# Kernel optimization log

Measured on AMD Instinct MI355X. Metric: run time of the kernel, lower is better.

Reference implementation:

```python
import jax, jax.numpy as jnp
import numpy as np


def _relative_position_index(ws: int) -> np.ndarray:
    # Matches torch meshgrid (ij) construction in _init_relative_positions.
    coords = np.stack(np.meshgrid(np.arange(ws), np.arange(ws), indexing='ij'), axis=0).reshape(2, -1)  # [2, ws*ws]
    rel = coords[:, :, None] - coords[:, None, :]          # [2, N, N]
    rel = rel.transpose(1, 2, 0).copy()                    # [N, N, 2]
    rel[:, :, 0] += ws - 1
    rel[:, :, 1] += ws - 1
    rel[:, :, 0] *= 2 * ws - 1
    return rel.sum(-1)                                     # [N, N] int


def setup_inputs() -> dict:
    key = jax.random.key(0)
    ks = jax.random.split(key, 6)
    B, N, C, H, WS = 4096, 49, 512, 16, 7
    x = jax.random.normal(ks[0], (B, N, C), dtype=jnp.float32)
    w_qkv = jax.random.normal(ks[1], (C, 3 * C), dtype=jnp.float32) * (C ** -0.5)
    b_qkv = jax.random.normal(ks[2], (3 * C,), dtype=jnp.float32) * 0.02
    w_proj = jax.random.normal(ks[3], (C, C), dtype=jnp.float32) * (C ** -0.5)
    b_proj = jax.random.normal(ks[4], (C,), dtype=jnp.float32) * 0.02
    bias_table = jax.random.normal(ks[5], ((2 * WS - 1) ** 2, H), dtype=jnp.float32) * 0.02
    return {"x": x, "w_qkv": w_qkv, "b_qkv": b_qkv, "w_proj": w_proj,
            "b_proj": b_proj, "bias_table": bias_table,
            "num_heads": H, "window_size": WS}


def reference(x, w_qkv, b_qkv, w_proj, b_proj, bias_table, num_heads, window_size):
    B, N, C = x.shape
    hd = C // num_heads
    qkv = (x @ w_qkv + b_qkv).reshape(B, N, 3, num_heads, hd)
    q, k, v = (qkv[:, :, i].transpose(0, 2, 1, 3) for i in range(3))  # each [B, H, N, hd]
    # NOTE: scale uses full channel dim C (as in source), not head_dim.
    attn = jnp.einsum('bhnd,bhmd->bhnm', q, k) * (C ** -0.5)          # [B, H, N, N]
    idx = _relative_position_index(window_size)                        # [N, N] static
    rel_bias = bias_table[idx].transpose(2, 0, 1)                      # [H, N, N]
    attn = jax.nn.softmax(attn + rel_bias[None], axis=-1)
    out = jnp.einsum('bhnm,bhmd->bhnd', attn, v)                       # [B, H, N, hd]
    out = out.transpose(0, 2, 1, 3).reshape(B, N, C)
    return out @ w_proj + b_proj
```

## Files before the change

### kernel.cpp

```cpp
#include <hip/hip_runtime.h>
#include <hip/hip_bf16.h>

typedef __attribute__((ext_vector_type(8))) short bf16x8;
typedef __attribute__((ext_vector_type(4))) float f32x4;

#define DEVI __device__ __forceinline__

DEVI short f2bf(float f) {
  union { float f; unsigned u; } v; v.f = f;
  unsigned r = v.u + 0x7FFFu + ((v.u >> 16) & 1u);
  return (short)(r >> 16);
}

DEVI void gl16(const void* g, void* l) {
  __builtin_amdgcn_global_load_lds((const __attribute__((address_space(1))) unsigned*)g,
                                   (__attribute__((address_space(3))) unsigned*)l,
                                   16, 0, 0);
}

DEVI float exp2a(float x) { float r; asm("v_exp_f32 %0, %1" : "=v"(r) : "v"(x)); return r; }

DEVI unsigned pk2(float lo, float hi) {
  union { __hip_bfloat162 h; unsigned u; } v;
  float2 f; f.x = lo; f.y = hi;
  v.h = __float22bfloat162_rn(f);
  return v.u;
}

union U8 { unsigned u[4]; bf16x8 v; };
DEVI bf16x8 mk8(unsigned a, unsigned b, unsigned c, unsigned d) {
  U8 x; x.u[0]=a; x.u[1]=b; x.u[2]=c; x.u[3]=d; return x.v;
}


__global__ __launch_bounds__(256) void conv_x_k(const float* __restrict__ x,
                                                short* __restrict__ xb) {
  long i = (long)blockIdx.x * 256 + threadIdx.x;
  const float4* xf = (const float4*)x;
  float4 a = xf[i * 2], c = xf[i * 2 + 1];
  bf16x8 r;
  r[0] = f2bf(a.x); r[1] = f2bf(a.y); r[2] = f2bf(a.z); r[3] = f2bf(a.w);
  r[4] = f2bf(c.x); r[5] = f2bf(c.y); r[6] = f2bf(c.z); r[7] = f2bf(c.w);
  *(bf16x8*)(xb + i * 8) = r;
}

__global__ __launch_bounds__(256) void prep_k(const float* __restrict__ wq,
                                              const float* __restrict__ wp,
                                              const float* __restrict__ btab,
                                              short* __restrict__ wqT,
                                              short* __restrict__ wpT,
                                              float* __restrict__ biasT) {
  int bid = blockIdx.x;
  if (bid < 3072) {
    int i = bid * 256 + threadIdx.x;
    int n = i >> 9, k = i & 511;
    wqT[i] = f2bf(wq[k * 1536 + n]);
  } else if (bid < 4096) {
    int i = (bid - 3072) * 256 + threadIdx.x;
    int n = i >> 9, k = i & 511;
    wpT[i] = f2bf(wp[k * 512 + n]);
  } else {
    int i = (bid - 4096) * 256 + threadIdx.x;
    int h = i >> 12, m = (i >> 6) & 63, n = i & 63;
    float v;
    if (m >= 49) {
      v = -1e30f;
    } else {
      int nn = n > 48 ? 48 : n;
      int ni = nn / 7, nj = nn - ni * 7;
      int mi = m / 7,  mj = m - mi * 7;
      int idx = (ni - mi + 6) * 13 + (nj - mj + 6);
      v = btab[idx * 16 + h] * 1.4426950408889634f;
    }
    biasT[i] = v;
  }
}


template <int EPI>
__global__ __launch_bounds__(512, 2)
void gemm256(const short* __restrict__ A, const short* __restrict__ Bt,
             const float* __restrict__ bias, void* __restrict__ outp, int ctiles) {
  __shared__ short Ls[65536];

  const int nwg = gridDim.x;
  const int w = blockIdx.x;
  const int chunk = nwg >> 3;
  const int tid = (w & 7) * chunk + (w >> 3);
  const int rt = tid / ctiles, ct = tid % ctiles;
  const long m0 = (long)rt * 256;
  const int n0 = ct * 256;

  const int t = threadIdx.x;
  const int lane = t & 63;
  const int wv = t >> 6;
  const int wr = wv >> 2;
  const int wc = wv & 3;
  const int l15 = lane & 15, g = lane >> 4, g4 = g * 4;

  const int gch = (t & 3) ^ ((t >> 3) & 3);
  const short* Ag = A + (m0 + (t >> 2)) * 512 + gch * 8;
  const short* Bg = Bt + (long)(n0 + (t >> 2)) * 512 + gch * 8;

  const int cA = ((g ^ ((l15 >> 1) & 3))) * 8;
  const int rowA = (wr * 128 + l15) * 32;
  const int rowB = (wc * 64 + l15) * 32;

  f32x4 acc[8][4] = {};
  bf16x8 af[8], bfr[2];

#define STAGE_A(ktn, kh, bufn)                                         \
  { const short* s_ = Ag + (ktn) * 64 + (kh) * 32;                     \
    short* d_ = (bufn) + (kh) * 8192 + t * 8;                          \
    gl16(s_, d_); gl16(s_ + 128 * 512, d_ + 4096); }
#define STAGE_B(ktn, kh, bufn)                                         \
  { const short* s_ = Bg + (ktn) * 64 + (kh) * 32;                     \
    short* d_ = (bufn) + 16384 + (kh) * 8192 + t * 8;                  \
    gl16(s_, d_); gl16(s_ + 128 * 512, d_ + 4096); }
#define LOAD_AF(Ab, kh)                                                \
  _Pragma("unroll")                                                    \
  for (int mf = 0; mf < 8; ++mf)                                       \
    af[mf] = *(const bf16x8*)((Ab) + (kh) * 8192 + rowA + mf * 512 + cA);
#define LOAD_BF(Ab, kh, nh)                                            \
  bfr[0] = *(const bf16x8*)((Ab) + 16384 + (kh) * 8192 + rowB + ((nh) * 2) * 512 + cA); \
  bfr[1] = *(const bf16x8*)((Ab) + 16384 + (kh) * 8192 + rowB + ((nh) * 2 + 1) * 512 + cA);
#define MFMA16(nh)                                                     \
  __builtin_amdgcn_s_setprio(1);                                       \
  _Pragma("unroll")                                                    \
  for (int mf = 0; mf < 8; ++mf) {                                     \
    acc[mf][(nh) * 2] = __builtin_amdgcn_mfma_f32_16x16x32_bf16(af[mf], bfr[0], acc[mf][(nh) * 2], 0, 0, 0);         \
    acc[mf][(nh) * 2 + 1] = __builtin_amdgcn_mfma_f32_16x16x32_bf16(af[mf], bfr[1], acc[mf][(nh) * 2 + 1], 0, 0, 0); \
  }                                                                    \
  __builtin_amdgcn_s_setprio(0);
#define BAR() asm volatile("s_barrier" ::: "memory")
#define VMW4() asm volatile("s_waitcnt vmcnt(4)" ::: "memory")

  STAGE_A(0, 0, Ls); STAGE_B(0, 0, Ls); STAGE_A(0, 1, Ls); STAGE_B(0, 1, Ls);
  VMW4();
  BAR();

  for (int kt = 0; kt < 8; ++kt) {
    const short* Ab = Ls + (kt & 1) * 32768;
    short* Bn = Ls + ((kt & 1) ^ 1) * 32768;
    const int ktn = kt < 7 ? kt + 1 : 7;

    LOAD_AF(Ab, 0); LOAD_BF(Ab, 0, 0);
    STAGE_A(ktn, 0, Bn);
    BAR(); MFMA16(0); BAR();

    LOAD_BF(Ab, 0, 1);
    STAGE_B(ktn, 0, Bn);
    VMW4();
    BAR(); MFMA16(1); BAR();

    LOAD_AF(Ab, 1); LOAD_BF(Ab, 1, 0);
    STAGE_A(ktn, 1, Bn);
    BAR(); MFMA16(0); BAR();

    LOAD_BF(Ab, 1, 1);
    STAGE_B(ktn, 1, Bn);
    VMW4();
    BAR(); MFMA16(1); BAR();
  }

  if (EPI == 0) {
    __syncthreads();
#pragma unroll
    for (int mf = 0; mf < 8; ++mf)
#pragma unroll
      for (int r = 0; r < 4; ++r) {
        int lrow = wr * 128 + mf * 16 + g4 + r;
#pragma unroll
        for (int nf = 0; nf < 4; ++nf) {
          int lcol = wc * 64 + nf * 16 + l15;
          Ls[lrow * 256 + lcol] = f2bf(acc[mf][nf][r] + bias[n0 + lcol]);
        }
      }
    __syncthreads();
    short* qkv = (short*)outp;
    const int cq = n0 >> 8;
    const int ii = cq >> 1;
#pragma unroll
    for (int s = 0; s < 16; ++s) {
      int c = s * 512 + t;
      int row = c >> 5, sub = c & 31;
      int hl = sub >> 2, d0 = (sub & 3) * 8;
      int rg = (int)m0 + row;
      int b = rg / 49, n = rg - b * 49;
      int h = (cq & 1) * 8 + hl;
      long dst = (long)((b * 16 + h) * 3 + ii) * 1568 + n * 32 + d0;
      *(bf16x8*)(qkv + dst) = *(const bf16x8*)(Ls + row * 256 + hl * 32 + d0);
    }
  } else {
    __syncthreads();
    float* out = (float*)outp;
#pragma unroll
    for (int mf = 0; mf < 8; ++mf)
#pragma unroll
      for (int r = 0; r < 4; ++r) {
        long row = m0 + wr * 128 + mf * 16 + g4 + r;
#pragma unroll
        for (int nf = 0; nf < 4; ++nf) {
          int col = n0 + wc * 64 + nf * 16 + l15;
          out[row * 512 + col] = acc[mf][nf][r] + bias[col];
        }
      }
  }
#undef STAGE_A
#undef STAGE_B
#undef LOAD_AF
#undef LOAD_BF
#undef MFMA16
#undef BAR
#undef VMW4
}


__global__ __launch_bounds__(256, 3)
void attn49(const short* __restrict__ qkvb, const float* __restrict__ biasT,
            short* __restrict__ ao) {
  __shared__ short Vl[4][2048];

  const int t = threadIdx.x, lane = t & 63, wv = t >> 6;
  const int l15 = lane & 15, g = lane >> 4, g4 = g * 4;
  const int b = blockIdx.x >> 2;
  const int h = (blockIdx.x & 3) * 4 + wv;

  const short* qb = qkvb + (long)(b * 16 + h) * 3 * 1568;
  const short* kb = qb + 1568;
  const short* vb = kb + 1568;
  short* Vs = Vl[wv];

#pragma unroll
  for (int it = 0; it < 4; ++it) {
    int c = it * 64 + lane; c = c > 195 ? 195 : c;
    *(bf16x8*)(Vs + c * 8) = *(const bf16x8*)(vb + c * 8);
  }

  bf16x8 qf[4], kf[4];
#pragma unroll
  for (int i = 0; i < 4; ++i) {
    int row = i * 16 + l15; row = row > 48 ? 48 : row;
    kf[i] = *(const bf16x8*)(kb + row * 32 + g * 8);
    qf[i] = *(const bf16x8*)(qb + row * 32 + g * 8);
  }

  f32x4 s[4][4] = {};
#pragma unroll
  for (int i = 0; i < 4; ++i)
#pragma unroll
    for (int j = 0; j < 4; ++j)
      s[i][j] = __builtin_amdgcn_mfma_f32_16x16x32_bf16(kf[i], qf[j], s[i][j], 0, 0, 0);

  bf16x8 vf[2][2];
#pragma unroll
  for (int kt = 0; kt < 2; ++kt)
#pragma unroll
    for (int hi = 0; hi < 2; ++hi)
#pragma unroll
      for (int r = 0; r < 4; ++r) {
        int m = kt * 32 + hi * 16 + g4 + r;
        m = m > 48 ? 48 : m;
#pragma unroll
        for (int dt = 0; dt < 2; ++dt)
          vf[kt][dt][hi * 4 + r] = Vs[m * 32 + dt * 16 + l15];
      }

  const float* biasH = biasT + h * 4096;
  float sum[4] = {0.f, 0.f, 0.f, 0.f};
#pragma unroll
  for (int i = 0; i < 4; ++i)
#pragma unroll
    for (int r = 0; r < 4; ++r) {
      int m = i * 16 + g4 + r;
      const float* bp = biasH + m * 64 + l15;
#pragma unroll
      for (int j = 0; j < 4; ++j) {
        float p = exp2a(fmaf(s[i][j][r], 0.06375871f, bp[j * 16]));
        s[i][j][r] = p;
        sum[j] += p;
      }
    }
#pragma unroll
  for (int j = 0; j < 4; ++j) {
    sum[j] += __shfl_xor(sum[j], 16);
    sum[j] += __shfl_xor(sum[j], 32);
    sum[j] = 1.f / sum[j];
  }

  unsigned pk[4][4][2];
#pragma unroll
  for (int j = 0; j < 4; ++j)
#pragma unroll
    for (int i = 0; i < 4; ++i) {
      pk[j][i][0] = pk2(s[i][j][0] * sum[j], s[i][j][1] * sum[j]);
      pk[j][i][1] = pk2(s[i][j][2] * sum[j], s[i][j][3] * sum[j]);
    }

  f32x4 o[4][2] = {};
#pragma unroll
  for (int j = 0; j < 4; ++j) {
    bf16x8 a0 = mk8(pk[j][0][0], pk[j][0][1], pk[j][1][0], pk[j][1][1]);
    bf16x8 a1 = mk8(pk[j][2][0], pk[j][2][1], pk[j][3][0], pk[j][3][1]);
    o[j][0] = __builtin_amdgcn_mfma_f32_16x16x32_bf16(a0, vf[0][0], o[j][0], 0, 0, 0);
    o[j][0] = __builtin_amdgcn_mfma_f32_16x16x32_bf16(a1, vf[1][0], o[j][0], 0, 0, 0);
    o[j][1] = __builtin_amdgcn_mfma_f32_16x16x32_bf16(a0, vf[0][1], o[j][1], 0, 0, 0);
    o[j][1] = __builtin_amdgcn_mfma_f32_16x16x32_bf16(a1, vf[1][1], o[j][1], 0, 0, 0);
  }

#pragma unroll
  for (int j = 0; j < 4; ++j)
#pragma unroll
    for (int r = 0; r < 4; ++r) {
      int n = j * 16 + g4 + r;
      if (n < 49) {
        long off = ((long)b * 49 + n) * 512 + h * 32 + l15;
        ao[off]      = f2bf(o[j][0][r]);
        ao[off + 16] = f2bf(o[j][1][r]);
      }
    }
}


extern "C" void kernel_launch(void* const* d_in, const int* in_sizes, int n_in,
                              void* d_out, int out_size, void* d_ws, size_t ws_size,
                              hipStream_t stream) {
  (void)in_sizes; (void)n_in; (void)ws_size;
  const float* x      = (const float*)d_in[0];
  const float* w_qkv  = (const float*)d_in[1];
  const float* b_qkv  = (const float*)d_in[2];
  const float* w_proj = (const float*)d_in[3];
  const float* b_proj = (const float*)d_in[4];
  const float* btab   = (const float*)d_in[5];

  char* ws = (char*)d_ws;
  short* xb  = (short*)ws;
  short* wqT = (short*)(ws + 205520896L);
  short* wpT = (short*)(ws + 205520896L + 1572864L);
  short* qkv = (short*)(ws + 205520896L + 1572864L + 524288L);
  short* ao  = xb;
  float* biasT = (float*)d_out + (out_size - 65536);

  conv_x_k<<<50176, 256, 0, stream>>>(x, xb);
  prep_k  <<<4352, 256, 0, stream>>>(w_qkv, w_proj, btab, wqT, wpT, biasT);
  gemm256<0><<<4704, 512, 0, stream>>>(xb, wqT, b_qkv, (void*)qkv, 6);
  attn49  <<<16384, 256, 0, stream>>>(qkv, biasT, ao);
  gemm256<1><<<1568, 512, 0, stream>>>(ao, wpT, b_proj, d_out, 2);
}
```

Baseline: 881.4 us.

## Fuse fp32-to-bf16 conversion of x into QKV GEMM and preswizzle weights

Removes the separate conversion kernel that turned x into bf16. The QKV GEMM now loads fp32 x directly, converts it in registers and writes it to LDS. Weights are prepacked into an MFMA fragment layout so B operands come straight from global/L2 into registers, freeing LDS for A only. The main loop is restructured with register-staged A loads, fewer barriers and halved LDS buffers. In exchange the fp32 A loads double global traffic per tile, the staging uses more registers, and the occupancy hint of 2 is dropped.

```diff
diff --git a/kernel.cpp b/kernel.cpp
--- a/kernel.cpp
+++ b/kernel.cpp
@@ -5,17 +5,12 @@
 typedef __attribute__((ext_vector_type(4))) float f32x4;
 
 #define DEVI __device__ __forceinline__
+#define MFMA __builtin_amdgcn_mfma_f32_16x16x32_bf16
 
 DEVI short f2bf(float f) {
   union { float f; unsigned u; } v; v.f = f;
   unsigned r = v.u + 0x7FFFu + ((v.u >> 16) & 1u);
   return (short)(r >> 16);
-}
-
-DEVI void gl16(const void* g, void* l) {
-  __builtin_amdgcn_global_load_lds((const __attribute__((address_space(1))) unsigned*)g,
-                                   (__attribute__((address_space(3))) unsigned*)l,
-                                   16, 0, 0);
 }
 
 DEVI float exp2a(float x) { float r; asm("v_exp_f32 %0, %1" : "=v"(r) : "v"(x)); return r; }
@@ -32,33 +27,20 @@
   U8 x; x.u[0]=a; x.u[1]=b; x.u[2]=c; x.u[3]=d; return x.v;
 }
 
-
-__global__ __launch_bounds__(256) void conv_x_k(const float* __restrict__ x,
-                                                short* __restrict__ xb) {
-  long i = (long)blockIdx.x * 256 + threadIdx.x;
-  const float4* xf = (const float4*)x;
-  float4 a = xf[i * 2], c = xf[i * 2 + 1];
-  bf16x8 r;
-  r[0] = f2bf(a.x); r[1] = f2bf(a.y); r[2] = f2bf(a.z); r[3] = f2bf(a.w);
-  r[4] = f2bf(c.x); r[5] = f2bf(c.y); r[6] = f2bf(c.z); r[7] = f2bf(c.w);
-  *(bf16x8*)(xb + i * 8) = r;
-}
-
 __global__ __launch_bounds__(256) void prep_k(const float* __restrict__ wq,
                                               const float* __restrict__ wp,
                                               const float* __restrict__ btab,
-                                              short* __restrict__ wqT,
-                                              short* __restrict__ wpT,
+                                              short* __restrict__ wqP,
+                                              short* __restrict__ wpP,
                                               float* __restrict__ biasT) {
   int bid = blockIdx.x;
-  if (bid < 3072) {
-    int i = bid * 256 + threadIdx.x;
-    int n = i >> 9, k = i & 511;
-    wqT[i] = f2bf(wq[k * 1536 + n]);
-  } else if (bid < 4096) {
-    int i = (bid - 3072) * 256 + threadIdx.x;
-    int n = i >> 9, k = i & 511;
-    wpT[i] = f2bf(wp[k * 512 + n]);
+  if (bid < 4096) {
+    int i = (bid < 3072 ? bid : bid - 3072) * 256 + threadIdx.x;
+    int e = i & 7, lane = (i >> 3) & 63, kc = (i >> 9) & 15, cf = i >> 13;
+    int k = kc * 32 + (lane >> 4) * 8 + e;
+    int col = cf * 16 + (lane & 15);
+    if (bid < 3072) wqP[i] = f2bf(wq[k * 1536 + col]);
+    else            wpP[i] = f2bf(wp[k * 512 + col]);
   } else {
     int i = (bid - 4096) * 256 + threadIdx.x;
     int h = i >> 12, m = (i >> 6) & 63, n = i & 63;
@@ -77,9 +59,9 @@
 }
 
 
-template <int EPI>
-__global__ __launch_bounds__(512, 2)
-void gemm256(const short* __restrict__ A, const short* __restrict__ Bt,
+template <int EPI, bool AF32>
+__global__ __launch_bounds__(512)
+void gemm256(const void* __restrict__ Ap, const short* __restrict__ wB,
              const float* __restrict__ bias, void* __restrict__ outp, int ctiles) {
   __shared__ short Ls[65536];
 
@@ -99,68 +81,87 @@
   const int l15 = lane & 15, g = lane >> 4, g4 = g * 4;
 
   const int gch = (t & 3) ^ ((t >> 3) & 3);
-  const short* Ag = A + (m0 + (t >> 2)) * 512 + gch * 8;
-  const short* Bg = Bt + (long)(n0 + (t >> 2)) * 512 + gch * 8;
-
-  const int cA = ((g ^ ((l15 >> 1) & 3))) * 8;
+  const float* Agf = (const float*)Ap + (m0 + (t >> 2)) * 512 + gch * 8;
+  const short* Agh = (const short*)Ap + (m0 + (t >> 2)) * 512 + gch * 8;
+
+  const int cA = (g ^ ((l15 >> 1) & 3)) * 8;
   const int rowA = (wr * 128 + l15) * 32;
-  const int rowB = (wc * 64 + l15) * 32;
+
+  const short* wBb = wB + ((long)(ct * 16 + wc * 4) << 13) + lane * 8;
 
   f32x4 acc[8][4] = {};
-  bf16x8 af[8], bfr[2];
-
-#define STAGE_A(ktn, kh, bufn)                                         \
-  { const short* s_ = Ag + (ktn) * 64 + (kh) * 32;                     \
-    short* d_ = (bufn) + (kh) * 8192 + t * 8;                          \
-    gl16(s_, d_); gl16(s_ + 128 * 512, d_ + 4096); }
-#define STAGE_B(ktn, kh, bufn)                                         \
-  { const short* s_ = Bg + (ktn) * 64 + (kh) * 32;                     \
-    short* d_ = (bufn) + 16384 + (kh) * 8192 + t * 8;                  \
-    gl16(s_, d_); gl16(s_ + 128 * 512, d_ + 4096); }
-#define LOAD_AF(Ab, kh)                                                \
-  _Pragma("unroll")                                                    \
-  for (int mf = 0; mf < 8; ++mf)                                       \
-    af[mf] = *(const bf16x8*)((Ab) + (kh) * 8192 + rowA + mf * 512 + cA);
-#define LOAD_BF(Ab, kh, nh)                                            \
-  bfr[0] = *(const bf16x8*)((Ab) + 16384 + (kh) * 8192 + rowB + ((nh) * 2) * 512 + cA); \
-  bfr[1] = *(const bf16x8*)((Ab) + 16384 + (kh) * 8192 + rowB + ((nh) * 2 + 1) * 512 + cA);
-#define MFMA16(nh)                                                     \
-  __builtin_amdgcn_s_setprio(1);                                       \
-  _Pragma("unroll")                                                    \
-  for (int mf = 0; mf < 8; ++mf) {                                     \
-    acc[mf][(nh) * 2] = __builtin_amdgcn_mfma_f32_16x16x32_bf16(af[mf], bfr[0], acc[mf][(nh) * 2], 0, 0, 0);         \
-    acc[mf][(nh) * 2 + 1] = __builtin_amdgcn_mfma_f32_16x16x32_bf16(af[mf], bfr[1], acc[mf][(nh) * 2 + 1], 0, 0, 0); \
-  }                                                                    \
+  bf16x8 af[8];
+  bf16x8 bP[4][2];
+  float4 ga[4][2];
+  bf16x8 gb[4];
+
+#define ISSUE_A(ktn)                                                          \
+  if (AF32) {                                                                 \
+    _Pragma("unroll")                                                         \
+    for (int c = 0; c < 4; ++c) {                                             \
+      const float* s_ = Agf + (c >> 1) * 65536 + (c & 1) * 32 + (ktn) * 64;   \
+      ga[c][0] = *(const float4*)s_;                                          \
+      ga[c][1] = *(const float4*)(s_ + 4);                                    \
+    }                                                                         \
+  } else {                                                                    \
+    _Pragma("unroll")                                                         \
+    for (int c = 0; c < 4; ++c)                                               \
+      gb[c] = *(const bf16x8*)(Agh + (c >> 1) * 65536 + (c & 1) * 32 + (ktn) * 64); \
+  }
+#define WRITE_A(nb)                                                           \
+  _Pragma("unroll")                                                           \
+  for (int c = 0; c < 4; ++c) {                                               \
+    short* d_ = (nb) + (c & 1) * 8192 + (c >> 1) * 4096 + t * 8;              \
+    if (AF32) {                                                               \
+      *(bf16x8*)d_ = mk8(pk2(ga[c][0].x, ga[c][0].y), pk2(ga[c][0].z, ga[c][0].w), \
+                         pk2(ga[c][1].x, ga[c][1].y), pk2(ga[c][1].z, ga[c][1].w)); \
+    } else {                                                                  \
+      *(bf16x8*)d_ = gb[c];                                                   \
+    }                                                                         \
+  }
+#define LOAD_BP(p, ktn)                                                       \
+  bP[p][0] = *(const bf16x8*)(wBb + ((((((p) & 1) * 2 + 0) * 16 + ((ktn) * 2 + ((p) >> 1)))) << 9)); \
+  bP[p][1] = *(const bf16x8*)(wBb + ((((((p) & 1) * 2 + 1) * 16 + ((ktn) * 2 + ((p) >> 1)))) << 9));
+#define LOAD_AF(buf, kh)                                                      \
+  _Pragma("unroll")                                                           \
+  for (int mf = 0; mf < 8; ++mf)                                              \
+    af[mf] = *(const bf16x8*)((buf) + (kh) * 8192 + rowA + mf * 512 + cA);
+#define MFMA16(p)                                                             \
+  __builtin_amdgcn_s_setprio(1);                                              \
+  _Pragma("unroll")                                                           \
+  for (int mf = 0; mf < 8; ++mf) {                                            \
+    acc[mf][((p) & 1) * 2]     = MFMA(af[mf], bP[p][0], acc[mf][((p) & 1) * 2], 0, 0, 0);     \
+    acc[mf][((p) & 1) * 2 + 1] = MFMA(af[mf], bP[p][1], acc[mf][((p) & 1) * 2 + 1], 0, 0, 0); \
+  }                                                                           \
   __builtin_amdgcn_s_setprio(0);
 #define BAR() asm volatile("s_barrier" ::: "memory")
-#define VMW4() asm volatile("s_waitcnt vmcnt(4)" ::: "memory")
-
-  STAGE_A(0, 0, Ls); STAGE_B(0, 0, Ls); STAGE_A(0, 1, Ls); STAGE_B(0, 1, Ls);
-  VMW4();
+
+  ISSUE_A(0);
+  asm volatile("s_waitcnt vmcnt(0)" ::: "memory");
+  WRITE_A(Ls);
+  LOAD_BP(0, 0); LOAD_BP(1, 0); LOAD_BP(2, 0); LOAD_BP(3, 0);
+  asm volatile("s_waitcnt lgkmcnt(0)" ::: "memory");
   BAR();
 
   for (int kt = 0; kt < 8; ++kt) {
-    const short* Ab = Ls + (kt & 1) * 32768;
-    short* Bn = Ls + ((kt & 1) ^ 1) * 32768;
-    const int ktn = kt < 7 ? kt + 1 : 7;
-
-    LOAD_AF(Ab, 0); LOAD_BF(Ab, 0, 0);
-    STAGE_A(ktn, 0, Bn);
-    BAR(); MFMA16(0); BAR();
-
-    LOAD_BF(Ab, 0, 1);
-    STAGE_B(ktn, 0, Bn);
-    VMW4();
-    BAR(); MFMA16(1); BAR();
-
-    LOAD_AF(Ab, 1); LOAD_BF(Ab, 1, 0);
-    STAGE_A(ktn, 1, Bn);
-    BAR(); MFMA16(0); BAR();
-
-    LOAD_BF(Ab, 1, 1);
-    STAGE_B(ktn, 1, Bn);
-    VMW4();
-    BAR(); MFMA16(1); BAR();
+    const short* buf = Ls + (kt & 1) * 16384;
+    short* nb = Ls + ((kt & 1) ^ 1) * 16384;
+
+    LOAD_AF(buf, 0);
+    if (kt < 7) ISSUE_A(kt + 1);
+    MFMA16(0);
+    MFMA16(1);
+    LOAD_AF(buf, 1);
+    if (kt < 7) { LOAD_BP(0, kt + 1); LOAD_BP(1, kt + 1); }
+    MFMA16(2);
+    if (kt < 7) {
+      asm volatile("s_waitcnt vmcnt(4)" ::: "memory");
+      WRITE_A(nb);
+    }
+    MFMA16(3);
+    if (kt < 7) { LOAD_BP(2, kt + 1); LOAD_BP(3, kt + 1); }
+    asm volatile("s_waitcnt lgkmcnt(0)" ::: "memory");
+    BAR();
   }
 
   if (EPI == 0) {
@@ -192,7 +193,6 @@
       *(bf16x8*)(qkv + dst) = *(const bf16x8*)(Ls + row * 256 + hl * 32 + d0);
     }
   } else {
-    __syncthreads();
     float* out = (float*)outp;
 #pragma unroll
     for (int mf = 0; mf < 8; ++mf)
@@ -206,13 +206,12 @@
         }
       }
   }
-#undef STAGE_A
-#undef STAGE_B
+#undef ISSUE_A
+#undef WRITE_A
+#undef LOAD_BP
 #undef LOAD_AF
-#undef LOAD_BF
 #undef MFMA16
 #undef BAR
-#undef VMW4
 }
 
 
@@ -250,7 +249,7 @@
   for (int i = 0; i < 4; ++i)
 #pragma unroll
     for (int j = 0; j < 4; ++j)
-      s[i][j] = __builtin_amdgcn_mfma_f32_16x16x32_bf16(kf[i], qf[j], s[i][j], 0, 0, 0);
+      s[i][j] = MFMA(kf[i], qf[j], s[i][j], 0, 0, 0);
 
   bf16x8 vf[2][2];
 #pragma unroll
@@ -302,10 +301,10 @@
   for (int j = 0; j < 4; ++j) {
     bf16x8 a0 = mk8(pk[j][0][0], pk[j][0][1], pk[j][1][0], pk[j][1][1]);
     bf16x8 a1 = mk8(pk[j][2][0], pk[j][2][1], pk[j][3][0], pk[j][3][1]);
-    o[j][0] = __builtin_amdgcn_mfma_f32_16x16x32_bf16(a0, vf[0][0], o[j][0], 0, 0, 0);
-    o[j][0] = __builtin_amdgcn_mfma_f32_16x16x32_bf16(a1, vf[1][0], o[j][0], 0, 0, 0);
-    o[j][1] = __builtin_amdgcn_mfma_f32_16x16x32_bf16(a0, vf[0][1], o[j][1], 0, 0, 0);
-    o[j][1] = __builtin_amdgcn_mfma_f32_16x16x32_bf16(a1, vf[1][1], o[j][1], 0, 0, 0);
+    o[j][0] = MFMA(a0, vf[0][0], o[j][0], 0, 0, 0);
+    o[j][0] = MFMA(a1, vf[1][0], o[j][0], 0, 0, 0);
+    o[j][1] = MFMA(a0, vf[0][1], o[j][1], 0, 0, 0);
+    o[j][1] = MFMA(a1, vf[1][1], o[j][1], 0, 0, 0);
   }
 
 #pragma unroll
@@ -334,16 +333,14 @@
   const float* btab   = (const float*)d_in[5];
 
   char* ws = (char*)d_ws;
-  short* xb  = (short*)ws;
-  short* wqT = (short*)(ws + 205520896L);
-  short* wpT = (short*)(ws + 205520896L + 1572864L);
-  short* qkv = (short*)(ws + 205520896L + 1572864L + 524288L);
-  short* ao  = xb;
+  short* wqP = (short*)ws;
+  short* wpP = (short*)(ws + 1572864L);
+  short* qkv = (short*)(ws + 2097152L);
+  short* ao  = (short*)(ws + 2097152L + 616562688L);
   float* biasT = (float*)d_out + (out_size - 65536);
 
-  conv_x_k<<<50176, 256, 0, stream>>>(x, xb);
-  prep_k  <<<4352, 256, 0, stream>>>(w_qkv, w_proj, btab, wqT, wpT, biasT);
-  gemm256<0><<<4704, 512, 0, stream>>>(xb, wqT, b_qkv, (void*)qkv, 6);
-  attn49  <<<16384, 256, 0, stream>>>(qkv, biasT, ao);
-  gemm256<1><<<1568, 512, 0, stream>>>(ao, wpT, b_proj, d_out, 2);
-}
+  prep_k<<<4352, 256, 0, stream>>>(w_qkv, w_proj, btab, wqP, wpP, biasT);
+  gemm256<0, true><<<4704, 512, 0, stream>>>(x, wqP, b_qkv, (void*)qkv, 6);
+  attn49<<<16384, 256, 0, stream>>>(qkv, biasT, ao);
+  gemm256<1, false><<<1568, 512, 0, stream>>>(ao, wpP, b_proj, d_out, 2);
+}
```

Result: faster. 852.6 us (median of 2 runs) (-3.3%).
